# Kernel tuning notes

Measured on AMD Instinct MI355X. Metric: run time of the kernel, lower is better.

The kernel has to match this reference:

```python
import jax, jax.numpy as jnp
import numpy as np

B, S, D, H, W = 4, 9, 256, 32, 32
RATIO = 2
NH = 16
DK = D // NH            # 16 (module recomputes d_k = d_in // n_head)
HP, WP = H // RATIO, W // RATIO
QL = H * W              # 1024 query tokens
KL = S * HP * WP        # 2304 key/value tokens


def setup_inputs() -> dict:
    key = jax.random.key(0)
    ks = jax.random.split(key, 8)
    s = 0.02
    return {
        "x": jax.random.normal(ks[0], (B, S, D, H, W), jnp.float32),
        "conv_w": jax.random.normal(ks[1], (D, D, RATIO, RATIO), jnp.float32) * s,
        "conv_b": jnp.zeros((D,), jnp.float32),
        "gn_g": jnp.ones((D,), jnp.float32),
        "gn_b": jnp.zeros((D,), jnp.float32),
        "wq": jax.random.normal(ks[2], (D, NH * DK), jnp.float32) * s,
        "bq": jnp.zeros((NH * DK,), jnp.float32),
        "wkv": jax.random.normal(ks[3], (D, 2 * NH * DK), jnp.float32) * s,
        "bkv": jnp.zeros((2 * NH * DK,), jnp.float32),
        "pos_bias": jax.random.normal(ks[4], (NH, QL, KL), jnp.float32) * s,
        "proj_w": jax.random.normal(ks[5], (D, D), jnp.float32) * s,
        "proj_b": jnp.zeros((D,), jnp.float32),
    }


def reference(x, conv_w, conv_b, gn_g, gn_b, wq, bq, wkv, bkv, pos_bias, proj_w, proj_b):
    b, s, d, h, w = x.shape
    hp, wp = h // RATIO, w // RATIO

    # query stream: center frame, flattened -> (b, h*w, d)
    v_self = x[:, 4].reshape(b, d, h * w).transpose(0, 2, 1)

    # key/value stream: Conv2d(k=stride=ratio) + GroupNorm(NH groups) over all frames
    vn = x.reshape(b * s, d, h, w)
    vn = jax.lax.conv_general_dilated(
        vn, conv_w, window_strides=(RATIO, RATIO), padding="VALID",
        dimension_numbers=("NCHW", "OIHW", "NCHW"))
    vn = vn + conv_b[None, :, None, None]
    g = vn.reshape(b * s, NH, d // NH, hp, wp)
    mu = g.mean(axis=(2, 3, 4), keepdims=True)
    var = g.var(axis=(2, 3, 4), keepdims=True)
    g = (g - mu) * jax.lax.rsqrt(var + 1e-5)
    vn = g.reshape(b * s, d, hp, wp) * gn_g[None, :, None, None] + gn_b[None, :, None, None]
    # (b, s*hp*wp, d)
    vn = vn.reshape(b, s, d, hp, wp).transpose(0, 1, 3, 4, 2).reshape(b, s * hp * wp, d)

    # projections
    q = (v_self @ wq + bq).reshape(b, h * w, NH, DK)            # (b, Q, H, dk)
    kv = (vn @ wkv + bkv).reshape(b, -1, 2, NH, DK)             # (b, K, 2, H, dk)
    k, v = kv[:, :, 0], kv[:, :, 1]                             # (b, K, H, dk)

    # cross-attention with learned positional bias added to QK^T
    dots = jnp.einsum("bqhd,bkhd->hbqk", q, k) * (DK ** -0.5)
    dots = dots + pos_bias[:, None]                             # (H, b, Q, K)
    attn = jax.nn.softmax(dots, axis=-1)
    out = jnp.einsum("hbqk,bkhd->bqhd", attn, v)                # (b, Q, H, dk)
    out = out.reshape(b, h, w, NH * DK)                         # (n c) head-major
    out = out @ proj_w + proj_b                                 # (b, h, w, d)

    # SpatialVit: 'b h w c -> b c h w'
    return out.transpose(0, 3, 1, 2)
```

## Files before the change

### kernel.cpp

```cpp
#include <hip/hip_runtime.h>

#define NBATCH 4
#define NSEQ   9
#define ND     256
#define NHEAD  16
#define NDKv   16
#define NQ     1024
#define NKL    2304
#define NKLH   1152
#define NSAMP  36

constexpr long OFF_CONV = 0;
constexpr long OFF_VN   = 2359296;
constexpr long OFF_WT   = 3538944;
constexpr long OFF_Q    = 4718592;
constexpr long OFF_K    = 5242880;
constexpr long OFF_VT   = 6422528;
constexpr long OFF_AO   = 0;
constexpr long OFF_PN   = 1048576;
constexpr long OFF_PL   = 3145728;

using bf16x8 = __attribute__((ext_vector_type(8))) short;
using f32x4  = __attribute__((ext_vector_type(4))) float;

__device__ __forceinline__ float bf2f(unsigned short h) {
    unsigned int u = ((unsigned int)h) << 16;
    float f; __builtin_memcpy(&f, &u, 4); return f;
}
__device__ __forceinline__ unsigned short f2bf(float f) {
    unsigned int u; __builtin_memcpy(&u, &f, 4);
    u += 0x7fffu + ((u >> 16) & 1u);
    return (unsigned short)(u >> 16);
}
__device__ __forceinline__ unsigned int cvtpk_bf16(float a, float b) {
    unsigned int r;
    asm("v_cvt_pk_bf16_f32 %0, %1, %2" : "=v"(r) : "v"(a), "v"(b));
    return r;
}
template<bool BF> __device__ __forceinline__ float ld1(const void* p, long i) {
    if constexpr (BF) return bf2f(((const unsigned short*)p)[i]);
    else return ((const float*)p)[i];
}
template<bool BF> __device__ __forceinline__ float4 ld4(const void* p, long i) {
    if constexpr (BF) { ushort4 v = *(const ushort4*)((const unsigned short*)p + i);
                        return make_float4(bf2f(v.x), bf2f(v.y), bf2f(v.z), bf2f(v.w)); }
    else return *(const float4*)((const float*)p + i);
}
template<bool BF> __device__ __forceinline__ void st1(void* p, long i, float v) {
    if constexpr (BF) ((unsigned short*)p)[i] = f2bf(v);
    else ((float*)p)[i] = v;
}
__device__ __forceinline__ bool detect_bf16(const void* gn_g) {
    return (*(const unsigned int*)gn_g) != 0x3F800000u;
}

template<bool BF>
__device__ void conv_body(const void* __restrict__ x, const void* __restrict__ cw,
                          const void* __restrict__ cb, float* __restrict__ ws) {
    __shared__ short lA[64 * 40];
    __shared__ short lB[128 * 40];
    const int tid  = threadIdx.x;
    const int n    = blockIdx.x;
    const int pq   = blockIdx.y;
    const int och  = blockIdx.z;
    const int wave = tid >> 6, lane = tid & 63;
    const int col  = lane & 15, quad = lane >> 4;

    f32x4 acc[4][2];
    #pragma unroll
    for (int mt = 0; mt < 4; ++mt)
        #pragma unroll
        for (int nt = 0; nt < 2; ++nt) acc[mt][nt] = {0.f, 0.f, 0.f, 0.f};

    const int icl  = tid >> 5;
    const int t5   = tid & 31;
    const int ihl  = t5 >> 2;
    const int iwg  = (t5 & 3) * 8;
    const int k0x  = icl * 4 + (ihl & 1) * 2;
    const int posx = (ihl >> 1) * 16 + (iwg >> 1);
    const long xrow = ((long)n * ND * 32 + (long)(pq * 8 + ihl)) * 32 + iwg;

    const int ocw = tid >> 3;
    const int kkw = (tid & 7) * 4;

    for (int kc = 0; kc < 32; ++kc) {
        __syncthreads();
        {
            const long xa = xrow + (long)(kc * 8 + icl) * 1024;
            float4 v0 = ld4<BF>(x, xa);
            float4 v1 = ld4<BF>(x, xa + 4);
            unsigned short us[8] = {f2bf(v0.x), f2bf(v0.y), f2bf(v0.z), f2bf(v0.w),
                                    f2bf(v1.x), f2bf(v1.y), f2bf(v1.z), f2bf(v1.w)};
            #pragma unroll
            for (int o = 0; o < 4; ++o)
                *(ushort2*)&lA[(posx + o) * 40 + k0x] = make_ushort2(us[2*o], us[2*o+1]);
        }
        #pragma unroll
        for (int j = 0; j < 4; ++j) {
            const int oc = ocw + j * 32;
            float4 wv = ld4<BF>(cw, (long)(och * 128 + oc) * 1024 + kc * 32 + kkw);
            unsigned int lo = (unsigned int)f2bf(wv.x) | ((unsigned int)f2bf(wv.y) << 16);
            unsigned int hi = (unsigned int)f2bf(wv.z) | ((unsigned int)f2bf(wv.w) << 16);
            *(uint2*)&lB[oc * 40 + kkw] = make_uint2(lo, hi);
        }
        __syncthreads();
        bf16x8 af[4];
        #pragma unroll
        for (int mt = 0; mt < 4; ++mt)
            af[mt] = *(const bf16x8*)&lA[(mt * 16 + col) * 40 + quad * 8];
        #pragma unroll
        for (int nt = 0; nt < 2; ++nt) {
            bf16x8 bfg = *(const bf16x8*)&lB[((wave * 2 + nt) * 16 + col) * 40 + quad * 8];
            #pragma unroll
            for (int mt = 0; mt < 4; ++mt)
                acc[mt][nt] = __builtin_amdgcn_mfma_f32_16x16x32_bf16(af[mt], bfg, acc[mt][nt], 0, 0, 0);
        }
    }

    float* co = ws + OFF_CONV + (long)n * 65536;
    #pragma unroll
    for (int nt = 0; nt < 2; ++nt) {
        const int oc = och * 128 + (wave * 2 + nt) * 16 + col;
        const float cbv = ld1<BF>(cb, oc);
        #pragma unroll
        for (int mt = 0; mt < 4; ++mt)
            #pragma unroll
            for (int r = 0; r < 4; ++r) {
                const int pos = pq * 64 + mt * 16 + quad * 4 + r;
                co[(long)pos * 256 + oc] = acc[mt][nt][r] + cbv;
            }
    }
}
__global__ void __launch_bounds__(256)
conv_k(const void* x, const void* cw, const void* cb, const void* gg, float* ws) {
    if (detect_bf16(gg)) conv_body<true>(x, cw, cb, ws);
    else                 conv_body<false>(x, cw, cb, ws);
}

template<bool BF>
__device__ void gn_body(const void* __restrict__ gn_g, const void* __restrict__ gn_b,
                        float* __restrict__ ws) {
    const int t = threadIdx.x;
    const int n = blockIdx.x;
    const int g = blockIdx.y;
    const float* row = ws + OFF_CONV + ((long)n * 256 + t) * 256 + g * 16;

    float v[16]; float s1 = 0.f, s2 = 0.f;
    #pragma unroll
    for (int q4 = 0; q4 < 4; ++q4) {
        float4 a = *(const float4*)(row + q4 * 4);
        v[q4*4+0] = a.x; v[q4*4+1] = a.y; v[q4*4+2] = a.z; v[q4*4+3] = a.w;
        s1 += (a.x + a.y) + (a.z + a.w);
        s2 += (a.x*a.x + a.y*a.y) + (a.z*a.z + a.w*a.w);
    }
    __shared__ float r1[4], r2[4];
    #pragma unroll
    for (int off = 32; off > 0; off >>= 1) {
        s1 += __shfl_down(s1, off, 64);
        s2 += __shfl_down(s2, off, 64);
    }
    if ((t & 63) == 0) { r1[t >> 6] = s1; r2[t >> 6] = s2; }
    __syncthreads();
    const float ts1 = r1[0] + r1[1] + r1[2] + r1[3];
    const float ts2 = r2[0] + r2[1] + r2[2] + r2[3];
    const float mean = ts1 * (1.0f / 4096.0f);
    const float var  = ts2 * (1.0f / 4096.0f) - mean * mean;
    const float inv  = rsqrtf(var + 1e-5f);

    const int b = n / NSEQ, s = n % NSEQ;
    float o[16];
    #pragma unroll
    for (int cl = 0; cl < 16; ++cl) {
        float gg = ld1<BF>(gn_g, g * 16 + cl);
        float bb = ld1<BF>(gn_b, g * 16 + cl);
        o[cl] = (v[cl] - mean) * inv * gg + bb;
    }
    unsigned short* dst = (unsigned short*)(ws + OFF_VN)
                          + ((long)b * NKL + s * 256 + t) * ND + g * 16;
    bf16x8 w0, w1;
    #pragma unroll
    for (int cl = 0; cl < 8; ++cl) {
        w0[cl] = (short)f2bf(o[cl]);
        w1[cl] = (short)f2bf(o[cl + 8]);
    }
    *(bf16x8*)dst       = w0;
    *(bf16x8*)(dst + 8) = w1;
}
__global__ void gn_k(const void* gg, const void* gb, float* ws) {
    if (detect_bf16(gg)) gn_body<true>(gg, gb, ws);
    else                 gn_body<false>(gg, gb, ws);
}

template<bool BF>
__device__ void tw_body(const void* __restrict__ wkv, float* __restrict__ ws) {
    __shared__ float tile[16][17];
    const int t = threadIdx.x;
    const int oc0 = blockIdx.x * 16;
    const int r = t >> 4, c = t & 15;
    unsigned short* wt = (unsigned short*)(ws + OFF_WT);
    for (int k0 = 0; k0 < ND; k0 += 16) {
        const float v = ld1<BF>(wkv, (long)(k0 + r) * 512 + oc0 + c);
        __syncthreads();
        tile[r][c] = v;
        __syncthreads();
        wt[(long)(oc0 + r) * ND + k0 + c] = f2bf(tile[c][r]);
    }
}
__global__ void __launch_bounds__(256)
tw_k(const void* wkv, const void* gg, float* ws) {
    if (detect_bf16(gg)) tw_body<true>(wkv, ws);
    else                 tw_body<false>(wkv, ws);
}

template<bool BF>
__device__ void q_body(const void* __restrict__ x, const void* __restrict__ wq,
                       const void* __restrict__ bq, float* __restrict__ ws) {
    const int lane = threadIdx.x;
    const int mb = blockIdx.x;
    const int ob = blockIdx.y;
    const int b  = mb >> 6;
    const int q0 = (mb & 63) * 16;
    const int oc = ob * 64 + lane;

    float acc[16];
    const float bqv = ld1<BF>(bq, oc);
    #pragma unroll
    for (int i = 0; i < 16; ++i) acc[i] = bqv;

    const long xoff = ((long)(b * NSEQ + 4) * ND) * NQ;
    for (int d = 0; d < ND; ++d) {
        const float wv = ld1<BF>(wq, (long)d * 256 + oc);
        const long vb = xoff + (long)d * NQ + q0;
        float4 a0 = ld4<BF>(x, vb + 0);
        float4 a1 = ld4<BF>(x, vb + 4);
        float4 a2 = ld4<BF>(x, vb + 8);
        float4 a3 = ld4<BF>(x, vb + 12);
        acc[0]  += a0.x * wv; acc[1]  += a0.y * wv; acc[2]  += a0.z * wv; acc[3]  += a0.w * wv;
        acc[4]  += a1.x * wv; acc[5]  += a1.y * wv; acc[6]  += a1.z * wv; acc[7]  += a1.w * wv;
        acc[8]  += a2.x * wv; acc[9]  += a2.y * wv; acc[10] += a2.z * wv; acc[11] += a2.w * wv;
        acc[12] += a3.x * wv; acc[13] += a3.y * wv; acc[14] += a3.z * wv; acc[15] += a3.w * wv;
    }
    const int h = oc >> 4, dk = oc & 15;
    unsigned short* qb = (unsigned short*)(ws + OFF_Q);
    #pragma unroll
    for (int i = 0; i < 16; ++i)
        qb[(((long)b * NHEAD + h) * NQ + q0 + i) * NDKv + dk] = f2bf(acc[i]);
}
__global__ void __launch_bounds__(64, 4)
q_k(const void* x, const void* wq, const void* bq, const void* gg, float* ws) {
    if (detect_bf16(gg)) q_body<true>(x, wq, bq, ws);
    else                 q_body<false>(x, wq, bq, ws);
}

template<bool BF>
__device__ void kv_body(const void* __restrict__ bkv, float* __restrict__ ws) {
    __shared__ short lA[64 * 32];
    __shared__ short lB[128 * 32];
    const int tid = threadIdx.x;
    const int b   = blockIdx.x / 36;
    const int t0  = (blockIdx.x % 36) * 64;
    const int ob  = blockIdx.y;
    const int wave = tid >> 6, lane = tid & 63;
    const int col = lane & 15, quad = lane >> 4;

    const unsigned short* vnb = (const unsigned short*)(ws + OFF_VN) + ((long)b * NKL + t0) * ND;
    const unsigned short* wtb = (const unsigned short*)(ws + OFF_WT) + (long)ob * 128 * ND;

    const int rS = tid >> 2;
    const int sS = (tid & 3) * 8;

    f32x4 acc[4][2];
    #pragma unroll
    for (int mt = 0; mt < 4; ++mt)
        #pragma unroll
        for (int nt = 0; nt < 2; ++nt) acc[mt][nt] = {0.f, 0.f, 0.f, 0.f};

    for (int kc = 0; kc < 8; ++kc) {
        __syncthreads();
        *(bf16x8*)&lA[rS * 32 + sS] =
            *(const bf16x8*)(vnb + (long)rS * ND + kc * 32 + sS);
        *(bf16x8*)&lB[rS * 32 + sS] =
            *(const bf16x8*)(wtb + (long)rS * ND + kc * 32 + sS);
        *(bf16x8*)&lB[(64 + rS) * 32 + sS] =
            *(const bf16x8*)(wtb + (long)(64 + rS) * ND + kc * 32 + sS);
        __syncthreads();
        bf16x8 af[4];
        #pragma unroll
        for (int mt = 0; mt < 4; ++mt)
            af[mt] = *(const bf16x8*)&lA[(mt * 16 + col) * 32 + quad * 8];
        #pragma unroll
        for (int nt = 0; nt < 2; ++nt) {
            bf16x8 bfg = *(const bf16x8*)&lB[((wave * 2 + nt) * 16 + col) * 32 + quad * 8];
            #pragma unroll
            for (int mt = 0; mt < 4; ++mt)
                acc[mt][nt] = __builtin_amdgcn_mfma_f32_16x16x32_bf16(af[mt], bfg, acc[mt][nt], 0, 0, 0);
        }
    }

    const bool isv = (ob >= 2);
    unsigned short* k16  = (unsigned short*)(ws + OFF_K);
    unsigned short* vt16 = (unsigned short*)(ws + OFF_VT);
    #pragma unroll
    for (int nt = 0; nt < 2; ++nt) {
        const int ocl = (wave * 2 + nt) * 16 + col;
        const int oc  = ob * 128 + ocl;
        const float bv = ld1<BF>(bkv, oc);
        const int oc2 = oc & 255, h = oc2 >> 4, dk = oc2 & 15;
        if (!isv) {
            #pragma unroll
            for (int mt = 0; mt < 4; ++mt)
                #pragma unroll
                for (int r = 0; r < 4; ++r) {
                    const int tok = t0 + mt * 16 + quad * 4 + r;
                    k16[((long)(b * NHEAD + h) * NKL + tok) * NDKv + dk] = f2bf(acc[mt][nt][r] + bv);
                }
        } else {
            #pragma unroll
            for (int mt = 0; mt < 4; ++mt) {
                const int tok = t0 + mt * 16 + quad * 4;
                ushort4 pk;
                pk.x = f2bf(acc[mt][nt][0] + bv);
                pk.y = f2bf(acc[mt][nt][1] + bv);
                pk.z = f2bf(acc[mt][nt][2] + bv);
                pk.w = f2bf(acc[mt][nt][3] + bv);
                *(ushort4*)&vt16[((long)(b * NHEAD + h) * 16 + dk) * NKL + tok] = pk;
            }
        }
    }
}
__global__ void __launch_bounds__(256)
kv_k(const void* bkv, const void* gg, float* ws) {
    if (detect_bf16(gg)) kv_body<true>(bkv, ws);
    else                 kv_body<false>(bkv, ws);
}

template<bool BF>
__device__ void attn_body(const void* __restrict__ pos_bias, float* __restrict__ ws) {
    __shared__ short plds[4 * 16 * 40];
    __shared__ float biasl[2][16 * 192];
    const int tid  = threadIdx.x;
    const int b    = tid >> 6;
    const int lane = tid & 63;
    const int qt   = blockIdx.x;
    const int h    = blockIdx.y;
    const int half = blockIdx.z;
    const int t0   = half * NKLH;
    const int bh = b * NHEAD + h;
    const int col  = lane & 15;
    const int quad = lane >> 4;
    short* myl = &plds[b * 640];

    const unsigned short* Qb = (const unsigned short*)(ws + OFF_Q);
    const unsigned short* Kb = (const unsigned short*)(ws + OFF_K);
    const unsigned short* Vt = (const unsigned short*)(ws + OFF_VT);

    bf16x8 qfrag = {0,0,0,0,0,0,0,0};
    if (quad < 2)
        qfrag = *(const bf16x8*)(Qb + (((long)bh * NQ + qt * 16 + col) * 16 + quad * 8));

    const unsigned short* Krows = Kb + ((long)bh * NKL + t0) * 16 + (long)col * 16 + (quad & 1) * 8;
    const unsigned short* Vrow  = Vt + ((long)bh * 16 + col) * NKL + t0 + quad * 8;

    f32x4 oacc = {0.f, 0.f, 0.f, 0.f};
    const f32x4 zc = {0.f, 0.f, 0.f, 0.f};
    float lsum = 0.f;

    auto do_chunk = [&](bf16x8 ck0, bf16x8 ck1, bf16x8 cv, float4 cb0, float4 cb1) {
        f32x4 s0 = __builtin_amdgcn_mfma_f32_16x16x32_bf16(ck0, qfrag, zc, 0, 0, 0);
        f32x4 s1 = __builtin_amdgcn_mfma_f32_16x16x32_bf16(ck1, qfrag, zc, 0, 0, 0);
        float p0 = __expf(s0[0] * 0.25f + cb0.x);
        float p1 = __expf(s0[1] * 0.25f + cb0.y);
        float p2 = __expf(s0[2] * 0.25f + cb0.z);
        float p3 = __expf(s0[3] * 0.25f + cb0.w);
        float r0 = __expf(s1[0] * 0.25f + cb1.x);
        float r1 = __expf(s1[1] * 0.25f + cb1.y);
        float r2 = __expf(s1[2] * 0.25f + cb1.z);
        float r3 = __expf(s1[3] * 0.25f + cb1.w);
        lsum += ((p0 + p1) + (p2 + p3)) + ((r0 + r1) + (r2 + r3));
        *(uint2*)(&myl[col * 40 + quad * 4]) =
            make_uint2(cvtpk_bf16(p0, p1), cvtpk_bf16(p2, p3));
        *(uint2*)(&myl[col * 40 + 16 + quad * 4]) =
            make_uint2(cvtpk_bf16(r0, r1), cvtpk_bf16(r2, r3));
        bf16x8 pfrag = *(const bf16x8*)(&myl[col * 40 + quad * 8]);
        oacc = __builtin_amdgcn_mfma_f32_16x16x32_bf16(pfrag, cv, oacc, 0, 0, 0);
    };

    if constexpr (BF) {
        const long pbase = ((long)h * NQ + qt * 16 + col) * NKL + t0 + quad * 4;
        bf16x8 kf0 = *(const bf16x8*)(Krows);
        bf16x8 kf1 = *(const bf16x8*)(Krows + 16L * 16);
        bf16x8 vf  = *(const bf16x8*)(Vrow);
        float4 pbA0 = ld4<BF>(pos_bias, pbase);
        float4 pbA1 = ld4<BF>(pos_bias, pbase + 16);
        float4 pbB0 = ld4<BF>(pos_bias, pbase + 32);
        float4 pbB1 = ld4<BF>(pos_bias, pbase + 48);
        for (int kb = 0; kb < NKLH; kb += 64) {
            {
                const bf16x8 ck0 = kf0, ck1 = kf1, cv = vf;
                const float4 cb0 = pbA0, cb1 = pbA1;
                const int nk = kb + 32;
                kf0 = *(const bf16x8*)(Krows + (long)nk * 16);
                kf1 = *(const bf16x8*)(Krows + (long)(nk + 16) * 16);
                vf  = *(const bf16x8*)(Vrow + nk);
                const int pk = (kb + 64 < NKLH) ? kb + 64 : 0;
                pbA0 = ld4<BF>(pos_bias, pbase + pk);
                pbA1 = ld4<BF>(pos_bias, pbase + pk + 16);
                do_chunk(ck0, ck1, cv, cb0, cb1);
            }
            {
                const bf16x8 ck0 = kf0, ck1 = kf1, cv = vf;
                const float4 cb0 = pbB0, cb1 = pbB1;
                const int nk = (kb + 64 < NKLH) ? kb + 64 : 0;
                kf0 = *(const bf16x8*)(Krows + (long)nk * 16);
                kf1 = *(const bf16x8*)(Krows + (long)(nk + 16) * 16);
                vf  = *(const bf16x8*)(Vrow + nk);
                const int pk = (kb + 96 < NKLH) ? kb + 96 : 0;
                pbB0 = ld4<BF>(pos_bias, pbase + pk);
                pbB1 = ld4<BF>(pos_bias, pbase + pk + 16);
                do_chunk(ck0, ck1, cv, cb0, cb1);
            }
        }
    } else {
        const int srow = tid >> 4;
        const int sseg = tid & 15;
        const long growbase = ((long)h * NQ + qt * 16 + srow) * NKL + t0;
        const int swz_st = (srow & 7) << 2;
        const int sw0 = (sseg * 4) ^ swz_st;
        const int swz_rd = (col & 7) << 2;

        {
            float4 a0 = ld4<false>(pos_bias, growbase + sseg * 4);
            float4 a1 = ld4<false>(pos_bias, growbase + sseg * 4 + 64);
            float4 a2 = ld4<false>(pos_bias, growbase + sseg * 4 + 128);
            float* dst = &biasl[0][srow * 192];
            *(float4*)&dst[sw0]       = a0;
            *(float4*)&dst[sw0 + 64]  = a1;
            *(float4*)&dst[sw0 + 128] = a2;
        }
        __syncthreads();

        bf16x8 kf0 = *(const bf16x8*)(Krows);
        bf16x8 kf1 = *(const bf16x8*)(Krows + 16L * 16);
        bf16x8 vf  = *(const bf16x8*)(Vrow);

        for (int ci = 0; ci < 6; ++ci) {
            float4 a0, a1, a2;
            if (ci < 5) {
                const long g = growbase + (ci + 1) * 192 + sseg * 4;
                a0 = ld4<false>(pos_bias, g);
                a1 = ld4<false>(pos_bias, g + 64);
                a2 = ld4<false>(pos_bias, g + 128);
            }
            const float* bb = &biasl[ci & 1][col * 192];
            #pragma unroll
            for (int sub = 0; sub < 6; ++sub) {
                const int kb = ci * 192 + sub * 32;
                const bf16x8 ck0 = kf0, ck1 = kf1, cv = vf;
                const int nk = (kb + 32 < NKLH) ? kb + 32 : 0;
                kf0 = *(const bf16x8*)(Krows + (long)nk * 16);
                kf1 = *(const bf16x8*)(Krows + (long)(nk + 16) * 16);
                vf  = *(const bf16x8*)(Vrow + nk);
                const int kl = sub * 32 + quad * 4;
                float4 cb0 = *(const float4*)&bb[kl ^ swz_rd];
                float4 cb1 = *(const float4*)&bb[(kl + 16) ^ swz_rd];
                do_chunk(ck0, ck1, cv, cb0, cb1);
            }
            if (ci < 5) {
                float* dst = &biasl[(ci + 1) & 1][srow * 192];
                *(float4*)&dst[sw0]       = a0;
                *(float4*)&dst[sw0 + 64]  = a1;
                *(float4*)&dst[sw0 + 128] = a2;
                __syncthreads();
            }
        }
    }

    lsum += __shfl_xor(lsum, 16, 64);
    lsum += __shfl_xor(lsum, 32, 64);

    float* pn = ws + OFF_PN + ((((long)half * NBATCH + b) * NHEAD + h) * NQ + qt * 16) * 16;
    #pragma unroll
    for (int r = 0; r < 4; ++r)
        pn[(long)(quad * 4 + r) * 16 + col] = oacc[r];
    if (quad == 0) {
        float* pl = ws + OFF_PL + (((long)half * NBATCH + b) * NHEAD + h) * NQ + qt * 16;
        pl[col] = lsum;
    }
}
__global__ void __launch_bounds__(256)
attn_k(const void* pos_bias, const void* gg, float* ws) {
    if (detect_bf16(gg)) attn_body<true>(pos_bias, ws);
    else                 attn_body<false>(pos_bias, ws);
}

__global__ void __launch_bounds__(256)
comb_k(float* __restrict__ ws) {
    const int idx = blockIdx.x * 256 + threadIdx.x;
    const int b   = idx >> 18;
    const int rem = idx & 262143;
    const int q   = rem >> 8;
    const int c   = rem & 255;
    const int h   = c >> 4, dv = c & 15;
    const float* pn = ws + OFF_PN;
    const float* pl = ws + OFF_PL;
    const long base0 = (((long)b * NHEAD + h) * NQ + q);
    const long base1 = ((((long)NBATCH + b) * NHEAD + h) * NQ + q);
    const float n = pn[base0 * 16 + dv] + pn[base1 * 16 + dv];
    const float l = pl[base0] + pl[base1];
    ws[OFF_AO + idx] = n / l;
}

template<bool BF>
__device__ void proj_body(const void* __restrict__ pw, const void* __restrict__ pbias,
                          const float* __restrict__ ws, void* __restrict__ out) {
    const int lane = threadIdx.x;
    const int bp = blockIdx.x;
    const int cbk = blockIdx.y;
    const int b = bp >> 4;
    const int p = (bp & 15) * 64 + lane;
    const int c0 = cbk * 16;

    const float* ao = ws + OFF_AO + ((long)b * NQ + p) * ND;
    float acc[16];
    #pragma unroll
    for (int i = 0; i < 16; ++i) acc[i] = ld1<BF>(pbias, c0 + i);

    for (int j = 0; j < ND; j += 4) {
        const float4 av = *(const float4*)(ao + j);
        #pragma unroll
        for (int jj = 0; jj < 4; ++jj) {
            const float a = (jj == 0) ? av.x : (jj == 1) ? av.y : (jj == 2) ? av.z : av.w;
            #pragma unroll
            for (int i = 0; i < 16; ++i) {
                const float w = ld1<BF>(pw, (long)(j + jj) * ND + c0 + i);
                acc[i] += a * w;
            }
        }
    }
    #pragma unroll
    for (int i = 0; i < 16; ++i)
        st1<BF>(out, ((long)b * ND + c0 + i) * NQ + p, acc[i]);
}
__global__ void __launch_bounds__(64, 4)
proj_k(const void* pw, const void* pbias, const void* gg, const float* ws, void* out) {
    if (detect_bf16(gg)) proj_body<true>(pw, pbias, ws, out);
    else                 proj_body<false>(pw, pbias, ws, out);
}

extern "C" void kernel_launch(void* const* d_in, const int* in_sizes, int n_in,
                              void* d_out, int out_size, void* d_ws, size_t ws_size,
                              hipStream_t stream) {
    (void)in_sizes; (void)n_in; (void)out_size; (void)ws_size;
    const void* x   = d_in[0];
    const void* cw  = d_in[1];
    const void* cb  = d_in[2];
    const void* gg  = d_in[3];
    const void* gb  = d_in[4];
    const void* wq  = d_in[5];
    const void* bq  = d_in[6];
    const void* wkv = d_in[7];
    const void* bkv = d_in[8];
    const void* pb  = d_in[9];
    const void* pw  = d_in[10];
    const void* pbb = d_in[11];
    float* ws = (float*)d_ws;

    conv_k   <<<dim3(36, 4, 2), 256, 0, stream>>>(x, cw, cb, gg, ws);
    gn_k     <<<dim3(36, 16),   256, 0, stream>>>(gg, gb, ws);
    tw_k     <<<dim3(32),       256, 0, stream>>>(wkv, gg, ws);
    q_k      <<<dim3(256, 4),    64, 0, stream>>>(x, wq, bq, gg, ws);
    kv_k     <<<dim3(144, 4),   256, 0, stream>>>(bkv, gg, ws);
    attn_k   <<<dim3(64, 16, 2), 256, 0, stream>>>(pb, gg, ws);
    comb_k   <<<dim3(4096),     256, 0, stream>>>(ws);
    proj_k   <<<dim3(64, 16),    64, 0, stream>>>(pw, pbb, gg, ws, d_out);
}
```

Baseline: 466.7 us.

## Add dedicated producer wave to stream positional bias into shared memory

```diff
diff --git a/kernel.cpp b/kernel.cpp
--- a/kernel.cpp
+++ b/kernel.cpp
@@ -339,15 +339,52 @@
     __shared__ short plds[4 * 16 * 40];
     __shared__ float biasl[2][16 * 192];
     const int tid  = threadIdx.x;
-    const int b    = tid >> 6;
+    const int wv   = tid >> 6;
     const int lane = tid & 63;
     const int qt   = blockIdx.x;
     const int h    = blockIdx.y;
     const int half = blockIdx.z;
     const int t0   = half * NKLH;
-    const int bh = b * NHEAD + h;
     const int col  = lane & 15;
     const int quad = lane >> 4;
+
+    if constexpr (!BF) {
+        if (wv == 4) {
+            const int pr = lane >> 2;
+            const int ps = lane & 3;
+            const long gbase = ((long)h * NQ + qt * 16 + pr) * NKL + t0 + ps * 4;
+            const int swz = (pr & 7) << 2;
+            const float* pb = (const float*)pos_bias;
+            float4 v[12];
+            #pragma unroll
+            for (int j = 0; j < 12; ++j) v[j] = *(const float4*)(pb + gbase + j * 16);
+            {
+                float* dst = &biasl[0][pr * 192];
+                #pragma unroll
+                for (int j = 0; j < 12; ++j)
+                    *(float4*)&dst[(ps * 4 + j * 16) ^ swz] = v[j];
+            }
+            __syncthreads();
+            for (int ci = 0; ci < 6; ++ci) {
+                if (ci < 5) {
+                    #pragma unroll
+                    for (int j = 0; j < 12; ++j)
+                        v[j] = *(const float4*)(pb + gbase + (ci + 1) * 192 + j * 16);
+                    float* dst = &biasl[(ci + 1) & 1][pr * 192];
+                    #pragma unroll
+                    for (int j = 0; j < 12; ++j)
+                        *(float4*)&dst[(ps * 4 + j * 16) ^ swz] = v[j];
+                }
+                __syncthreads();
+            }
+            return;
+        }
+    } else {
+        if (wv == 4) return;
+    }
+
+    const int b  = wv;
+    const int bh = b * NHEAD + h;
     short* myl = &plds[b * 640];
 
     const unsigned short* Qb = (const unsigned short*)(ws + OFF_Q);
@@ -421,36 +458,14 @@
             }
         }
     } else {
-        const int srow = tid >> 4;
-        const int sseg = tid & 15;
-        const long growbase = ((long)h * NQ + qt * 16 + srow) * NKL + t0;
-        const int swz_st = (srow & 7) << 2;
-        const int sw0 = (sseg * 4) ^ swz_st;
         const int swz_rd = (col & 7) << 2;
-
-        {
-            float4 a0 = ld4<false>(pos_bias, growbase + sseg * 4);
-            float4 a1 = ld4<false>(pos_bias, growbase + sseg * 4 + 64);
-            float4 a2 = ld4<false>(pos_bias, growbase + sseg * 4 + 128);
-            float* dst = &biasl[0][srow * 192];
-            *(float4*)&dst[sw0]       = a0;
-            *(float4*)&dst[sw0 + 64]  = a1;
-            *(float4*)&dst[sw0 + 128] = a2;
-        }
-        __syncthreads();
 
         bf16x8 kf0 = *(const bf16x8*)(Krows);
         bf16x8 kf1 = *(const bf16x8*)(Krows + 16L * 16);
         bf16x8 vf  = *(const bf16x8*)(Vrow);
+        __syncthreads();
 
         for (int ci = 0; ci < 6; ++ci) {
-            float4 a0, a1, a2;
-            if (ci < 5) {
-                const long g = growbase + (ci + 1) * 192 + sseg * 4;
-                a0 = ld4<false>(pos_bias, g);
-                a1 = ld4<false>(pos_bias, g + 64);
-                a2 = ld4<false>(pos_bias, g + 128);
-            }
             const float* bb = &biasl[ci & 1][col * 192];
             #pragma unroll
             for (int sub = 0; sub < 6; ++sub) {
@@ -465,13 +480,7 @@
                 float4 cb1 = *(const float4*)&bb[(kl + 16) ^ swz_rd];
                 do_chunk(ck0, ck1, cv, cb0, cb1);
             }
-            if (ci < 5) {
-                float* dst = &biasl[(ci + 1) & 1][srow * 192];
-                *(float4*)&dst[sw0]       = a0;
-                *(float4*)&dst[sw0 + 64]  = a1;
-                *(float4*)&dst[sw0 + 128] = a2;
-                __syncthreads();
-            }
+            __syncthreads();
         }
     }
 
@@ -487,7 +496,7 @@
         pl[col] = lsum;
     }
 }
-__global__ void __launch_bounds__(256)
+__global__ void __launch_bounds__(320)
 attn_k(const void* pos_bias, const void* gg, float* ws) {
     if (detect_bf16(gg)) attn_body<true>(pos_bias, ws);
     else                 attn_body<false>(pos_bias, ws);
@@ -570,7 +579,7 @@
     tw_k     <<<dim3(32),       256, 0, stream>>>(wkv, gg, ws);
     q_k      <<<dim3(256, 4),    64, 0, stream>>>(x, wq, bq, gg, ws);
     kv_k     <<<dim3(144, 4),   256, 0, stream>>>(bkv, gg, ws);
-    attn_k   <<<dim3(64, 16, 2), 256, 0, stream>>>(pb, gg, ws);
+    attn_k   <<<dim3(64, 16, 2), 320, 0, stream>>>(pb, gg, ws);
     comb_k   <<<dim3(4096),     256, 0, stream>>>(ws);
     proj_k   <<<dim3(64, 16),    64, 0, stream>>>(pw, pbb, gg, ws, d_out);
 }
```

Result: slower. 476.3 us (+2.1%).
